# Optimization experiments

Measured on AMD Instinct MI355X. Metric: run time of the kernel, lower is better.

The kernel has to match this reference:

```python
import jax, jax.numpy as jnp
import numpy as np

EMBED = 1024
HEAD = 64

def setup_inputs() -> dict:
    key = jax.random.key(0)
    k1, k2, k3, k4 = jax.random.split(key, 4)
    # Torch Linear weight layout: [out_features, in_features]; xavier_uniform init
    bound = float(np.sqrt(6.0 / (EMBED + HEAD)))
    embeddings = jax.random.normal(k1, (4, 4096, EMBED), dtype=jnp.float32)
    W_Q = jax.random.uniform(k2, (HEAD, EMBED), dtype=jnp.float32, minval=-bound, maxval=bound)
    W_K = jax.random.uniform(k3, (HEAD, EMBED), dtype=jnp.float32, minval=-bound, maxval=bound)
    W_V = jax.random.uniform(k4, (HEAD, EMBED), dtype=jnp.float32, minval=-bound, maxval=bound)
    return {"embeddings": embeddings, "W_Q": W_Q, "W_K": W_K, "W_V": W_V}

def reference(embeddings, W_Q, W_K, W_V):
    # embeddings: [B, S, E]; weights: [H, E] (torch Linear layout, y = x @ W.T)
    B, S, E = embeddings.shape
    H = W_Q.shape[0]
    Q = jnp.einsum('bse,he->bsh', embeddings, W_Q)
    K = jnp.einsum('bse,he->bsh', embeddings, W_K)
    V = jnp.einsum('bse,he->bsh', embeddings, W_V)
    scale = 1.0 / jnp.sqrt(jnp.float32(H))
    scores = jnp.einsum('bqh,bkh->bqk', Q, K) * scale  # [B, S, S]
    causal = jnp.tril(jnp.ones((S, S), dtype=bool))
    scores = jnp.where(causal, scores, -jnp.inf)
    attn = jax.nn.softmax(scores, axis=-1)
    # dropout (p=0.1) is identity at inference; omitted for determinism
    return jnp.einsum('bqk,bkh->bqh', attn, V)  # [B, S, H]
```

## Files before the change

### kernel.cpp

```cpp
#include <hip/hip_runtime.h>
#include <hip/hip_bf16.h>

#define EMBED 1024
#define SEQ   4096
#define NBATCH 4
#define HD    64
#define CH    8
#define NP    8

typedef __attribute__((ext_vector_type(8))) short s16x8;
typedef __attribute__((ext_vector_type(4))) float f32x4;
typedef __attribute__((ext_vector_type(4))) unsigned int u32x4;

__device__ __forceinline__ short f2bf(float f) {
    unsigned u = __builtin_bit_cast(unsigned, f);
    u += 0x7fffu + ((u >> 16) & 1u);
    return (short)(u >> 16);
}

typedef const unsigned int __attribute__((address_space(1)))* gbl_ptr_t;
typedef unsigned int __attribute__((address_space(3)))* lds_ptr_t;
__device__ __forceinline__ void async16(const void* g, void* l) {
    __builtin_amdgcn_global_load_lds((gbl_ptr_t)g, (lds_ptr_t)l, 16, 0, 0);
}

__global__ __launch_bounds__(256) void prep_w(
    const float* __restrict__ wq, const float* __restrict__ wk,
    const float* __restrict__ wv, short* __restrict__ Wb)
{
    int idx = blockIdx.x * 256 + threadIdx.x;
    int e = idx * 8;
    int row = e >> 10, col = e & 1023;
    const float* src = (row < 64) ? (wq + (size_t)row * EMBED)
                     : (row < 128) ? (wk + (size_t)(row - 64) * EMBED)
                                   : (wv + (size_t)(row - 128) * EMBED);
    float sc = (row < 64) ? 0.125f : 1.0f;
    float4 f0 = *(const float4*)(src + col);
    float4 f1 = *(const float4*)(src + col + 4);
    s16x8 v = { f2bf(f0.x*sc), f2bf(f0.y*sc), f2bf(f0.z*sc), f2bf(f0.w*sc),
                f2bf(f1.x*sc), f2bf(f1.y*sc), f2bf(f1.z*sc), f2bf(f1.w*sc) };
    *(s16x8*)&Wb[e] = v;
}

__global__ __launch_bounds__(256) void proj_qkv(
    const float* __restrict__ emb, const short* __restrict__ Wb,
    short* __restrict__ Qb, short* __restrict__ Kb, short* __restrict__ Vt)
{
    __shared__ short Alds[2][32 * 64];
    __shared__ short Blds[2][192 * 64];

    const int tid  = threadIdx.x;
    const int lane = tid & 63;
    const int w    = tid >> 6;
    const int wr   = w & 1;
    const int wc   = w >> 1;
    const int row0 = blockIdx.x * 32;

    const int sr   = tid >> 3;
    const int sg   = tid & 7;
    const int srow = lane >> 3;
    const int sblk = lane & 7;

    f32x4 acc[6];
#pragma unroll
    for (int i = 0; i < 6; ++i) acc[i] = f32x4{0.f, 0.f, 0.f, 0.f};

    auto stageB = [&](int buf, int t) {
        const int k0 = t * 64;
#pragma unroll
        for (int i = 0; i < 6; ++i) {
            int r = w * 48 + i * 8 + srow;
            async16(Wb + (size_t)r * EMBED + k0 + ((sblk ^ (r & 7)) * 8),
                    &Blds[buf][(w * 48 + i * 8) * 64]);
        }
    };
    const float* abase = emb + (size_t)(row0 + sr) * EMBED + sg * 8;
    auto writeA = [&](int buf, float4 f0, float4 f1) {
        s16x8 v = { f2bf(f0.x), f2bf(f0.y), f2bf(f0.z), f2bf(f0.w),
                    f2bf(f1.x), f2bf(f1.y), f2bf(f1.z), f2bf(f1.w) };
        *(s16x8*)&Alds[buf][sr * 64 + ((sg ^ (sr & 7)) * 8)] = v;
    };

    float4 f0a = *(const float4*)(abase);
    float4 f1a = *(const float4*)(abase + 4);
    stageB(0, 0);
    writeA(0, f0a, f1a);
    f0a = *(const float4*)(abase + 64);
    f1a = *(const float4*)(abase + 68);
    __syncthreads();

    int cur = 0;
    const int ar = wr * 16 + (lane & 15);
    const int ag = lane >> 4;
    float4 f0b = f0a, f1b = f1a;

    for (int t = 0; t < 16; ++t) {
        if (t < 14) {
            f0b = *(const float4*)(abase + (size_t)(t + 2) * 64);
            f1b = *(const float4*)(abase + (size_t)(t + 2) * 64 + 4);
        }
        if (t < 15) stageB(cur ^ 1, t + 1);

        s16x8 a0 = *(const s16x8*)&Alds[cur][ar * 64 + (((ag    ) ^ (ar & 7)) * 8)];
        s16x8 a1 = *(const s16x8*)&Alds[cur][ar * 64 + (((ag + 4) ^ (ar & 7)) * 8)];
#pragma unroll
        for (int n = 0; n < 6; ++n) {
            int br = wc * 96 + n * 16 + (lane & 15);
            s16x8 b0 = *(const s16x8*)&Blds[cur][br * 64 + (((ag    ) ^ (br & 7)) * 8)];
            s16x8 b1 = *(const s16x8*)&Blds[cur][br * 64 + (((ag + 4) ^ (br & 7)) * 8)];
            acc[n] = __builtin_amdgcn_mfma_f32_16x16x32_bf16(a0, b0, acc[n], 0, 0, 0);
            acc[n] = __builtin_amdgcn_mfma_f32_16x16x32_bf16(a1, b1, acc[n], 0, 0, 0);
        }
        if (t < 15) writeA(cur ^ 1, f0a, f1a);
        __syncthreads();
        f0a = f0b; f1a = f1b;
        cur ^= 1;
    }

    const int rbase = row0 + wr * 16 + ((lane >> 4) * 4);
    const int cl = lane & 15;
#pragma unroll
    for (int n = 0; n < 6; ++n) {
        int col = wc * 96 + n * 16 + cl;
        int mat = col >> 6;
        int c = col & 63;
#pragma unroll
        for (int r = 0; r < 4; ++r) {
            int row = rbase + r;
            int b = row >> 12, s = row & 4095;
            short v = f2bf(acc[n][r]);
            if (mat == 0)       Qb[((size_t)b * SEQ + s) * HD + c] = v;
            else if (mat == 1)  Kb[((size_t)b * SEQ + s) * HD + c] = v;
            else                Vt[((size_t)b * HD + c) * SEQ + s] = v;
        }
    }
}

__global__ __launch_bounds__(256) void attn_fwd(
    const short* __restrict__ Qb, const short* __restrict__ Kb,
    const short* __restrict__ Vt, float* __restrict__ Op, float* __restrict__ Ml)
{
    const int jq = 63 - blockIdx.x;
    const int b  = blockIdx.z;
    const int p  = blockIdx.y;
    const int t0 = p * CH;
    if (t0 > jq) return;
    const int t1 = min(t0 + CH, jq + 1);

    __shared__ short Qlds[64 * 64];
    __shared__ short Klds[2][64 * 64];
    __shared__ short Vlds[2][64 * 64];

    const int tid  = threadIdx.x;
    const int lane = tid & 63;
    const int w    = tid >> 6;
    const int l15  = lane & 15;
    const int g    = lane >> 4;
    const int q0w  = jq * 64 + w * 16;

    const short* Qbase  = Qb + ((size_t)b * SEQ + jq * 64) * HD;
    const short* Kbase0 = Kb + (size_t)b * SEQ * HD;
    const short* Vbase0 = Vt + (size_t)b * HD * SEQ;

    const int srow = lane >> 3;
    const int sblk = lane & 7;

    auto stageKV = [&](int buf, int t) {
        const int kv0 = t * 64;
#pragma unroll
        for (int i = 0; i < 2; ++i) {
            int r = w * 16 + i * 8 + srow;
            async16(Kbase0 + (size_t)(kv0 + r) * HD + ((sblk ^ (r & 7)) * 8),
                    &Klds[buf][(w * 16 + i * 8) * 64]);
            async16(Vbase0 + (size_t)r * SEQ + kv0 + ((sblk ^ (r & 7)) * 8),
                    &Vlds[buf][(w * 16 + i * 8) * 64]);
        }
    };

#pragma unroll
    for (int i = 0; i < 2; ++i) {
        int r = w * 16 + i * 8 + srow;
        async16(Qbase + (size_t)r * HD + ((sblk ^ (r & 7)) * 8),
                &Qlds[(w * 16 + i * 8) * 64]);
    }
    stageKV(0, t0);
    __syncthreads();

    const int qr = w * 16 + l15;
    s16x8 qb0 = *(const s16x8*)&Qlds[qr * 64 + (((g    ) ^ (qr & 7)) * 8)];
    s16x8 qb1 = *(const s16x8*)&Qlds[qr * 64 + (((g + 4) ^ (qr & 7)) * 8)];

    f32x4 o[4];
#pragma unroll
    for (int n = 0; n < 4; ++n) o[n] = f32x4{0.f, 0.f, 0.f, 0.f};
    float m = -INFINITY, l = 0.f;

    const int f1l = (2 * (g & 1) + (g >> 1)) * 16 + l15;
    const int f2l = (2 * (g & 1) + 1 - (g >> 1)) * 16 + l15;
    const bool podd = (g & 1) != 0;
    const bool hbit = (g >> 1) != 0;

    int cur = 0;
    for (int t = t0; t < t1; ++t) {
        if (t + 1 < t1) stageKV(cur ^ 1, t + 1);

        f32x4 st[4];
        __builtin_amdgcn_s_setprio(1);
#pragma unroll
        for (int n = 0; n < 4; ++n) {
            int kr = n * 16 + l15;
            s16x8 ka0 = *(const s16x8*)&Klds[cur][kr * 64 + (((g    ) ^ (kr & 7)) * 8)];
            s16x8 ka1 = *(const s16x8*)&Klds[cur][kr * 64 + (((g + 4) ^ (kr & 7)) * 8)];
            st[n] = __builtin_amdgcn_mfma_f32_16x16x32_bf16(ka0, qb0, f32x4{0.f,0.f,0.f,0.f}, 0, 0, 0);
            st[n] = __builtin_amdgcn_mfma_f32_16x16x32_bf16(ka1, qb1, st[n], 0, 0, 0);
        }
        __builtin_amdgcn_s_setprio(0);

        if (t == jq) {
#pragma unroll
            for (int n = 0; n < 4; ++n)
#pragma unroll
                for (int r = 0; r < 4; ++r) {
                    int kvg = t * 64 + n * 16 + g * 4 + r;
                    if (kvg > q0w + l15) st[n][r] = -INFINITY;
                }
        }

        float mt = fmaxf(fmaxf(st[0][0], st[0][1]), fmaxf(st[0][2], st[0][3]));
#pragma unroll
        for (int n = 1; n < 4; ++n)
            mt = fmaxf(mt, fmaxf(fmaxf(st[n][0], st[n][1]), fmaxf(st[n][2], st[n][3])));
        mt = fmaxf(mt, __shfl_xor(mt, 16, 64));
        mt = fmaxf(mt, __shfl_xor(mt, 32, 64));

        if (__any(mt - m > 8.f)) {
            float mn  = fmaxf(m, mt);
            float fac = __expf(m - mn);
            m = mn;
            l *= fac;
#pragma unroll
            for (int n = 0; n < 4; ++n)
#pragma unroll
                for (int r = 0; r < 4; ++r) o[n][r] *= fac;
        }

        float rs = 0.f;
        unsigned pk[4][2];
#pragma unroll
        for (int n = 0; n < 4; ++n) {
            float p0 = __expf(st[n][0] - m);
            float p1 = __expf(st[n][1] - m);
            float p2 = __expf(st[n][2] - m);
            float p3 = __expf(st[n][3] - m);
            rs += (p0 + p1) + (p2 + p3);
            asm("v_cvt_pk_bf16_f32 %0, %1, %2" : "=v"(pk[n][0]) : "v"(p0), "v"(p1));
            asm("v_cvt_pk_bf16_f32 %0, %1, %2" : "=v"(pk[n][1]) : "v"(p2), "v"(p3));
        }
        rs += __shfl_xor(rs, 16, 64);
        rs += __shfl_xor(rs, 32, 64);
        l += rs;

        __builtin_amdgcn_s_setprio(1);
#pragma unroll
        for (int kk = 0; kk < 2; ++kk) {
            unsigned e00 = podd ? pk[2 * kk + 1][0] : pk[2 * kk][0];
            unsigned e01 = podd ? pk[2 * kk + 1][1] : pk[2 * kk][1];
            unsigned e10 = podd ? pk[2 * kk][0]     : pk[2 * kk + 1][0];
            unsigned e11 = podd ? pk[2 * kk][1]     : pk[2 * kk + 1][1];
            unsigned x0 = (unsigned)__shfl((int)e00, f1l, 64);
            unsigned x1 = (unsigned)__shfl((int)e01, f1l, 64);
            unsigned y0 = (unsigned)__shfl((int)e10, f2l, 64);
            unsigned y1 = (unsigned)__shfl((int)e11, f2l, 64);
            unsigned w0 = hbit ? y0 : x0;
            unsigned w1 = hbit ? y1 : x1;
            unsigned w2 = hbit ? x0 : y0;
            unsigned w3 = hbit ? x1 : y1;
            u32x4 uu = { w0, w1, w2, w3 };
            s16x8 pb = __builtin_bit_cast(s16x8, uu);
#pragma unroll
            for (int n = 0; n < 4; ++n) {
                int vr = n * 16 + l15;
                s16x8 va = *(const s16x8*)&Vlds[cur][vr * 64 + (((g + kk * 4) ^ (vr & 7)) * 8)];
                o[n] = __builtin_amdgcn_mfma_f32_16x16x32_bf16(va, pb, o[n], 0, 0, 0);
            }
        }
        __builtin_amdgcn_s_setprio(0);
        __syncthreads();
        cur ^= 1;
    }

    const size_t pidx = ((size_t)b * 64 + jq) * NP + p;
    float* opb = Op + pidx * 4096;
#pragma unroll
    for (int n = 0; n < 4; ++n)
#pragma unroll
        for (int r = 0; r < 4; ++r)
            opb[(n * 16 + g * 4 + r) * 64 + w * 16 + l15] = o[n][r];
    if (lane < 16) {
        float* mlb = Ml + pidx * 128;
        mlb[w * 16 + l15]      = m;
        mlb[64 + w * 16 + l15] = l;
    }
}

__global__ __launch_bounds__(256) void attn_combine(
    const float* __restrict__ Op, const float* __restrict__ Ml,
    float* __restrict__ out)
{
    const int jq = blockIdx.x;
    const int b  = blockIdx.y;
    const int nP = (jq >> 3) + 1;
    const int tid = threadIdx.x;
    const int q  = tid & 63;
    const int dc = tid >> 6;
    const size_t pb = ((size_t)b * 64 + jq) * NP;

    float mv[NP], lv[NP], wt[NP];
    float mstar = -INFINITY;
#pragma unroll
    for (int p = 0; p < NP; ++p) if (p < nP) {
        mv[p] = Ml[(pb + p) * 128 + q];
        lv[p] = Ml[(pb + p) * 128 + 64 + q];
        mstar = fmaxf(mstar, mv[p]);
    }
    float L = 0.f;
#pragma unroll
    for (int p = 0; p < NP; ++p) if (p < nP) {
        wt[p] = __expf(mv[p] - mstar);
        L += lv[p] * wt[p];
    }
    float inv = 1.0f / L;

    float acc[16];
#pragma unroll
    for (int k = 0; k < 16; ++k) acc[k] = 0.f;
#pragma unroll
    for (int p = 0; p < NP; ++p) if (p < nP) {
        const float* src = Op + (pb + p) * 4096 + (size_t)dc * 16 * 64 + q;
#pragma unroll
        for (int k = 0; k < 16; ++k) acc[k] += src[k * 64] * wt[p];
    }
    float* dst = out + ((size_t)b * SEQ + jq * 64 + q) * HD + dc * 16;
#pragma unroll
    for (int k = 0; k < 16; ++k) dst[k] = acc[k] * inv;
}

extern "C" void kernel_launch(void* const* d_in, const int* in_sizes, int n_in,
                              void* d_out, int out_size, void* d_ws, size_t ws_size,
                              hipStream_t stream)
{
    (void)in_sizes; (void)n_in; (void)out_size; (void)ws_size;
    const float* emb = (const float*)d_in[0];
    const float* wq  = (const float*)d_in[1];
    const float* wk  = (const float*)d_in[2];
    const float* wv  = (const float*)d_in[3];
    float* out = (float*)d_out;

    short* Wb = (short*)d_ws;
    short* Qb = Wb + 192 * 1024;
    short* Kb = Qb + (size_t)NBATCH * SEQ * HD;
    short* Vt = Kb + (size_t)NBATCH * SEQ * HD;
    float* Op = (float*)(Vt + (size_t)NBATCH * SEQ * HD);
    float* Ml = Op + (size_t)NBATCH * 64 * NP * 64 * 64;

    hipLaunchKernelGGL(prep_w, dim3(96), dim3(256), 0, stream, wq, wk, wv, Wb);
    hipLaunchKernelGGL(proj_qkv, dim3(512), dim3(256), 0, stream, emb, Wb, Qb, Kb, Vt);
    hipLaunchKernelGGL(attn_fwd, dim3(64, NP, NBATCH), dim3(256), 0, stream,
                       Qb, Kb, Vt, Op, Ml);
    hipLaunchKernelGGL(attn_combine, dim3(64, NBATCH), dim3(256), 0, stream,
                       Op, Ml, out);
}
```

Before: 150.7 us.

## Deepen prefetch with explicit waitcnt barriers and compact attention grid

The projection GEMM and attention kernels now prefetch two stages ahead and use explicit s_waitcnt plus raw s_barrier instead of __syncthreads, so global loads stay in flight across barriers. The attention grid is compacted from 64x8 blocks with early exits to 288 valid (query-tile, partition) pairs per batch, decoded with a triangular index formula. Q is loaded directly into registers from global memory rather than staged through LDS. The hand-placed vmcnt counts and the index decoding are fragile and must exactly match the number of outstanding async loads.

```diff
diff --git a/kernel.cpp b/kernel.cpp
--- a/kernel.cpp
+++ b/kernel.cpp
@@ -87,20 +87,16 @@
     writeA(0, f0a, f1a);
     f0a = *(const float4*)(abase + 64);
     f1a = *(const float4*)(abase + 68);
-    __syncthreads();
+    stageB(1, 1);
+    asm volatile("s_waitcnt vmcnt(8) lgkmcnt(0)" ::: "memory");
+    __builtin_amdgcn_s_barrier();
+    __builtin_amdgcn_sched_barrier(0);
 
     int cur = 0;
     const int ar = wr * 16 + (lane & 15);
     const int ag = lane >> 4;
-    float4 f0b = f0a, f1b = f1a;
 
     for (int t = 0; t < 16; ++t) {
-        if (t < 14) {
-            f0b = *(const float4*)(abase + (size_t)(t + 2) * 64);
-            f1b = *(const float4*)(abase + (size_t)(t + 2) * 64 + 4);
-        }
-        if (t < 15) stageB(cur ^ 1, t + 1);
-
         s16x8 a0 = *(const s16x8*)&Alds[cur][ar * 64 + (((ag    ) ^ (ar & 7)) * 8)];
         s16x8 a1 = *(const s16x8*)&Alds[cur][ar * 64 + (((ag + 4) ^ (ar & 7)) * 8)];
 #pragma unroll
@@ -111,9 +107,21 @@
             acc[n] = __builtin_amdgcn_mfma_f32_16x16x32_bf16(a0, b0, acc[n], 0, 0, 0);
             acc[n] = __builtin_amdgcn_mfma_f32_16x16x32_bf16(a1, b1, acc[n], 0, 0, 0);
         }
-        if (t < 15) writeA(cur ^ 1, f0a, f1a);
-        __syncthreads();
-        f0a = f0b; f1a = f1b;
+        if (t == 15) break;
+
+        __builtin_amdgcn_s_barrier();
+        __builtin_amdgcn_sched_barrier(0);
+        writeA(cur ^ 1, f0a, f1a);
+        if (t < 14) {
+            f0a = *(const float4*)(abase + (size_t)(t + 2) * 64);
+            f1a = *(const float4*)(abase + (size_t)(t + 2) * 64 + 4);
+            stageB(cur, t + 2);
+            asm volatile("s_waitcnt vmcnt(8) lgkmcnt(0)" ::: "memory");
+        } else {
+            asm volatile("s_waitcnt vmcnt(0) lgkmcnt(0)" ::: "memory");
+        }
+        __builtin_amdgcn_s_barrier();
+        __builtin_amdgcn_sched_barrier(0);
         cur ^= 1;
     }
 
@@ -140,14 +148,18 @@
     const short* __restrict__ Qb, const short* __restrict__ Kb,
     const short* __restrict__ Vt, float* __restrict__ Op, float* __restrict__ Ml)
 {
-    const int jq = 63 - blockIdx.x;
-    const int b  = blockIdx.z;
-    const int p  = blockIdx.y;
+    const int b = blockIdx.y;
+    const int i = 287 - blockIdx.x;
+    int k = (int)((sqrtf((float)(16 + 16 * i)) - 4.0f) * 0.125f);
+    while (4 * (k + 1) * (k + 2) <= i) ++k;
+    while (4 * k * (k + 1) > i) --k;
+    const int rem = i - 4 * k * (k + 1);
+    const int kp1 = k + 1;
+    const int jq = 8 * k + rem / kp1;
+    const int p  = rem - (rem / kp1) * kp1;
     const int t0 = p * CH;
-    if (t0 > jq) return;
     const int t1 = min(t0 + CH, jq + 1);
 
-    __shared__ short Qlds[64 * 64];
     __shared__ short Klds[2][64 * 64];
     __shared__ short Vlds[2][64 * 64];
 
@@ -158,7 +170,6 @@
     const int g    = lane >> 4;
     const int q0w  = jq * 64 + w * 16;
 
-    const short* Qbase  = Qb + ((size_t)b * SEQ + jq * 64) * HD;
     const short* Kbase0 = Kb + (size_t)b * SEQ * HD;
     const short* Vbase0 = Vt + (size_t)b * HD * SEQ;
 
@@ -168,27 +179,28 @@
     auto stageKV = [&](int buf, int t) {
         const int kv0 = t * 64;
 #pragma unroll
-        for (int i = 0; i < 2; ++i) {
-            int r = w * 16 + i * 8 + srow;
+        for (int i2 = 0; i2 < 2; ++i2) {
+            int r = w * 16 + i2 * 8 + srow;
             async16(Kbase0 + (size_t)(kv0 + r) * HD + ((sblk ^ (r & 7)) * 8),
-                    &Klds[buf][(w * 16 + i * 8) * 64]);
+                    &Klds[buf][(w * 16 + i2 * 8) * 64]);
             async16(Vbase0 + (size_t)r * SEQ + kv0 + ((sblk ^ (r & 7)) * 8),
-                    &Vlds[buf][(w * 16 + i * 8) * 64]);
+                    &Vlds[buf][(w * 16 + i2 * 8) * 64]);
         }
     };
 
-#pragma unroll
-    for (int i = 0; i < 2; ++i) {
-        int r = w * 16 + i * 8 + srow;
-        async16(Qbase + (size_t)r * HD + ((sblk ^ (r & 7)) * 8),
-                &Qlds[(w * 16 + i * 8) * 64]);
-    }
+    const short* qp = Qb + ((size_t)b * SEQ + q0w + l15) * HD + g * 8;
+    s16x8 qb0 = *(const s16x8*)qp;
+    s16x8 qb1 = *(const s16x8*)(qp + 32);
+
     stageKV(0, t0);
-    __syncthreads();
-
-    const int qr = w * 16 + l15;
-    s16x8 qb0 = *(const s16x8*)&Qlds[qr * 64 + (((g    ) ^ (qr & 7)) * 8)];
-    s16x8 qb1 = *(const s16x8*)&Qlds[qr * 64 + (((g + 4) ^ (qr & 7)) * 8)];
+    if (t0 + 1 < t1) {
+        stageKV(1, t0 + 1);
+        asm volatile("s_waitcnt vmcnt(4)" ::: "memory");
+    } else {
+        asm volatile("s_waitcnt vmcnt(0)" ::: "memory");
+    }
+    __builtin_amdgcn_s_barrier();
+    __builtin_amdgcn_sched_barrier(0);
 
     f32x4 o[4];
 #pragma unroll
@@ -202,8 +214,6 @@
 
     int cur = 0;
     for (int t = t0; t < t1; ++t) {
-        if (t + 1 < t1) stageKV(cur ^ 1, t + 1);
-
         f32x4 st[4];
         __builtin_amdgcn_s_setprio(1);
 #pragma unroll
@@ -285,8 +295,20 @@
             }
         }
         __builtin_amdgcn_s_setprio(0);
-        __syncthreads();
-        cur ^= 1;
+
+        if (t + 1 < t1) {
+            __builtin_amdgcn_s_barrier();
+            __builtin_amdgcn_sched_barrier(0);
+            if (t + 2 < t1) {
+                stageKV(cur, t + 2);
+                asm volatile("s_waitcnt vmcnt(4)" ::: "memory");
+            } else {
+                asm volatile("s_waitcnt vmcnt(0)" ::: "memory");
+            }
+            __builtin_amdgcn_s_barrier();
+            __builtin_amdgcn_sched_barrier(0);
+            cur ^= 1;
+        }
     }
 
     const size_t pidx = ((size_t)b * 64 + jq) * NP + p;
@@ -333,16 +355,16 @@
 
     float acc[16];
 #pragma unroll
-    for (int k = 0; k < 16; ++k) acc[k] = 0.f;
+    for (int k2 = 0; k2 < 16; ++k2) acc[k2] = 0.f;
 #pragma unroll
     for (int p = 0; p < NP; ++p) if (p < nP) {
         const float* src = Op + (pb + p) * 4096 + (size_t)dc * 16 * 64 + q;
 #pragma unroll
-        for (int k = 0; k < 16; ++k) acc[k] += src[k * 64] * wt[p];
+        for (int k2 = 0; k2 < 16; ++k2) acc[k2] += src[k2 * 64] * wt[p];
     }
     float* dst = out + ((size_t)b * SEQ + jq * 64 + q) * HD + dc * 16;
 #pragma unroll
-    for (int k = 0; k < 16; ++k) dst[k] = acc[k] * inv;
+    for (int k2 = 0; k2 < 16; ++k2) dst[k2] = acc[k2] * inv;
 }
 
 extern "C" void kernel_launch(void* const* d_in, const int* in_sizes, int n_in,
@@ -365,7 +387,7 @@
 
     hipLaunchKernelGGL(prep_w, dim3(96), dim3(256), 0, stream, wq, wk, wv, Wb);
     hipLaunchKernelGGL(proj_qkv, dim3(512), dim3(256), 0, stream, emb, Wb, Qb, Kb, Vt);
-    hipLaunchKernelGGL(attn_fwd, dim3(64, NP, NBATCH), dim3(256), 0, stream,
+    hipLaunchKernelGGL(attn_fwd, dim3(288, NBATCH), dim3(256), 0, stream,
                        Qb, Kb, Vt, Op, Ml);
     hipLaunchKernelGGL(attn_combine, dim3(64, NBATCH), dim3(256), 0, stream,
                        Op, Ml, out);
```

Measured after the change: 150.3 us. About the same (-0.3%).
